# Kernel optimization log

Measured on AMD Instinct MI355X. Metric: run time of the kernel, lower is better.

Reference implementation:

```python
import jax, jax.numpy as jnp
import numpy as np

ANCHORS = np.array([[10,13],[16,30],[33,23],[30,61],[62,45],[59,119],[116,90],[156,198],[373,326]], dtype=np.float32)
ANCHOR_MASK = [[6,7,8],[3,4,5],[0,1,2]]
NUM_CLASSES = 80
IGNORE_THRESH = 0.5
MAX_BOXES = 32   # fixed padding replacing dynamic boolean-mask box extraction
BS = 16
GRIDS = [13, 26, 52]
NA = 3
INPUT = 416.0


def setup_inputs() -> dict:
    rng = np.random.default_rng(0)
    inp = {}
    for l, g in enumerate(GRIDS):
        inp[f"feats{l}"] = jnp.asarray(rng.normal(0.0, 0.5, size=(BS, NA * (5 + NUM_CLASSES), g, g)).astype(np.float32))
        yt = np.zeros((BS, g, g, NA, 5 + NUM_CLASSES), np.float32)
        n_obj = 20
        for b in range(BS):
            gy = rng.integers(0, g, n_obj); gx = rng.integers(0, g, n_obj); a = rng.integers(0, NA, n_obj)
            yt[b, gy, gx, a, 0:2] = rng.uniform(0.0, 1.0, (n_obj, 2)).astype(np.float32)
            yt[b, gy, gx, a, 2:4] = rng.uniform(0.05, 0.5, (n_obj, 2)).astype(np.float32)
            yt[b, gy, gx, a, 4] = 1.0
            cls = rng.integers(0, NUM_CLASSES, n_obj)
            yt[b, gy, gx, a, 5 + cls] = 1.0
        inp[f"ytrue{l}"] = jnp.asarray(yt)
    return inp


def _bce_logits(x, t):
    # BCEWithLogits (stable): softplus(x) - x*t
    return jax.nn.softplus(x) - x * t


def _pairwise_iou(b1, b2):
    # b1: [bs, N, 4] xywh, b2: [bs, M, 4] xywh -> [bs, N, M]
    b1 = b1[:, :, None, :]
    b2 = b2[:, None, :, :]
    b1_mins = b1[..., :2] - b1[..., 2:4] * 0.5
    b1_maxes = b1[..., :2] + b1[..., 2:4] * 0.5
    b2_mins = b2[..., :2] - b2[..., 2:4] * 0.5
    b2_maxes = b2[..., :2] + b2[..., 2:4] * 0.5
    inter_wh = jnp.clip(jnp.minimum(b1_maxes, b2_maxes) - jnp.maximum(b1_mins, b2_mins), 0.0)
    inter = inter_wh[..., 0] * inter_wh[..., 1]
    a1 = b1[..., 2] * b1[..., 3]
    a2 = b2[..., 2] * b2[..., 3]
    return inter / (a1 + a2 - inter)


def _layer_loss(feats, ytrue, anchors):
    bs, _, gh, gw = feats.shape
    C = 5 + NUM_CLASSES
    raw = feats.reshape(bs, NA, C, gh, gw).transpose(0, 3, 4, 1, 2)  # [bs,gh,gw,na,C]
    gy, gx = jnp.meshgrid(jnp.arange(gh), jnp.arange(gw), indexing="ij")
    grid = jnp.stack([gx, gy], axis=-1).astype(raw.dtype)[None, :, :, None, :]  # [1,gh,gw,1,2] (x,y)
    anchors_t = jnp.asarray(anchors, dtype=raw.dtype)                           # [na,2]
    gshape = jnp.array([gh, gw], raw.dtype)

    pred_xy = (jax.nn.sigmoid(raw[..., :2]) + grid) / gshape
    pred_wh = jnp.exp(raw[..., 2:4]) * anchors_t / INPUT
    pred_box = jnp.concatenate([pred_xy, pred_wh], axis=-1)  # [bs,gh,gw,na,4]

    obj = ytrue[..., 4:5]
    raw_true_xy = ytrue[..., :2] * gshape - grid
    safe_wh = jnp.where(obj > 0, ytrue[..., 2:4], anchors_t / INPUT)  # avoids log(0) off-object
    raw_true_wh = jnp.where(obj > 0, jnp.log(safe_wh / anchors_t * INPUT), 0.0)
    box_loss_scale = 2.0 - ytrue[..., 2:3] * ytrue[..., 3:4]

    # --- best-IoU ignore mask (padded, jit-static replacement for per-image boolean masking) ---
    N = gh * gw * NA
    pb = pred_box.reshape(bs, N, 4)
    obj_flat = obj.reshape(bs, N)
    boxes_flat = ytrue[..., :4].reshape(bs, N, 4)
    vals, idx = jax.lax.top_k(obj_flat, MAX_BOXES)                 # obj cells first
    true_boxes = jnp.take_along_axis(boxes_flat, idx[..., None], axis=1)  # [bs,MAXB,4]
    valid = vals > 0.5                                             # [bs,MAXB]
    iou = jnp.where(valid[:, None, :], _pairwise_iou(pb, true_boxes), 0.0)
    best_iou = jnp.max(iou, axis=2).reshape(bs, gh, gw, NA, 1)
    ignore = (best_iou < IGNORE_THRESH).astype(raw.dtype)

    xy_loss = jnp.sum(obj * box_loss_scale * _bce_logits(raw[..., 0:2], raw_true_xy)) / bs
    wh_loss = jnp.sum(obj * box_loss_scale * jnp.square(raw[..., 2:4] - raw_true_wh)) / bs
    conf_bce = _bce_logits(raw[..., 4:5], obj)
    conf_loss = jnp.sum(conf_bce * obj + (1.0 - obj) * conf_bce * ignore) / bs
    cls_loss = jnp.sum(obj * _bce_logits(raw[..., 5:], ytrue[..., 5:])) / bs
    return xy_loss, wh_loss, conf_loss, cls_loss


def reference(feats0, feats1, feats2, ytrue0, ytrue1, ytrue2):
    feats = [feats0, feats1, feats2]
    ytrue = [ytrue0, ytrue1, ytrue2]
    loss_xy = loss_wh = loss_conf = loss_cls = 0.0
    for l in range(3):
        xy, wh, cf, cl = _layer_loss(feats[l], ytrue[l], ANCHORS[ANCHOR_MASK[l]])
        loss_xy = loss_xy + xy
        loss_wh = loss_wh + wh
        loss_conf = loss_conf + cf
        loss_cls = loss_cls + cl
    total = loss_xy + loss_wh + loss_conf + loss_cls
    return (total[None], loss_xy[None], loss_wh[None], loss_conf[None], loss_cls[None])
```

## Files before the change

### kernel.cpp

```cpp
#include <hip/hip_runtime.h>

#define NCLS 80
#define REC  255
#define NA   3
#define BSZ  16
#define MAXB 32

#define G0 13
#define G1 26
#define G2 52
#define GG0 (G0*G0)
#define GG1 (G1*G1)
#define GG2 (G2*G2)
#define CELLS0 (BSZ*NA*GG0)
#define CELLS1 (BSZ*NA*GG1)
#define CELLS2 (BSZ*NA*GG2)
#define TOTAL  (CELLS0+CELLS1+CELLS2)

#define MB ((TOTAL+255)/256)
#define OB 240

__device__ const float d_anch[3][3][2] = {
  {{116.f, 90.f}, {156.f, 198.f}, {373.f, 326.f}},
  {{ 30.f, 61.f}, { 62.f,  45.f}, { 59.f, 119.f}},
  {{ 10.f, 13.f}, { 16.f,  30.f}, { 33.f,  23.f}},
};

__device__ inline float sp(float x) {
  return fmaxf(x, 0.0f) + log1pf(expf(-fabsf(x)));
}
__device__ inline float sigm(float x) { return 1.0f / (1.0f + expf(-x)); }
__device__ inline float wred(float v) {
  #pragma unroll
  for (int off = 32; off > 0; off >>= 1) v += __shfl_down(v, off, 64);
  return v;
}
__device__ inline float wmax(float v) {
  #pragma unroll
  for (int off = 32; off > 0; off >>= 1) v = fmaxf(v, __shfl_xor(v, off, 64));
  return v;
}

__device__ inline int cell_grp(int t) {
  if (t < CELLS0) {
    unsigned r = (unsigned)t / (unsigned)GG0; return (int)(r / 3u);
  } else if (t < CELLS0 + CELLS1) {
    unsigned r = (unsigned)(t - CELLS0) / (unsigned)GG1; return 16 + (int)(r / 3u);
  }
  unsigned r = (unsigned)(t - CELLS0 - CELLS1) / (unsigned)GG2; return 32 + (int)(r / 3u);
}

template<int L>
__device__ inline void gather_one(int idx, const float* __restrict__ yt,
                                  int* __restrict__ cnt, float* __restrict__ boxes,
                                  int* __restrict__ total, int* __restrict__ objlist) {
  constexpr int GG = (L == 0) ? GG0 : (L == 1) ? GG1 : GG2;
  unsigned rest = (unsigned)idx / (unsigned)GG;
  int cell = idx - (int)rest * GG;
  unsigned b = rest / 3u;
  int a = (int)(rest - b * 3u);
  size_t base = ((size_t)((int)b * GG + cell) * 3 + a) * 85;
  float obj = yt[base + 4];
  if (obj > 0.5f) {
    int grp = L * BSZ + (int)b;
    int p = atomicAdd(&cnt[grp], 1);
    if (p < MAXB) {
      float* d = boxes + (grp * MAXB + p) * 4;
      d[0] = yt[base]; d[1] = yt[base + 1]; d[2] = yt[base + 2]; d[3] = yt[base + 3];
    }
    int s = atomicAdd(total, 1);
    if (s < 1024) objlist[s] = (grp << 18) | (a << 16) | cell;
  }
}

__global__ __launch_bounds__(256)
void gather_kernel(const float* __restrict__ y0, const float* __restrict__ y1,
                   const float* __restrict__ y2, int* __restrict__ cnt,
                   float* __restrict__ boxes, int* __restrict__ total,
                   int* __restrict__ objlist) {
  int t = blockIdx.x * 256 + threadIdx.x;
  if (t >= TOTAL) return;
  if (t < CELLS0)               gather_one<0>(t,                   y0, cnt, boxes, total, objlist);
  else if (t < CELLS0 + CELLS1) gather_one<1>(t - CELLS0,          y1, cnt, boxes, total, objlist);
  else                          gather_one<2>(t - CELLS0 - CELLS1, y2, cnt, boxes, total, objlist);
}

template<int L>
__device__ inline float conf_cell(int idx, const float* __restrict__ fp,
                                  const float4* __restrict__ sbox,
                                  const int* __restrict__ scnt, int gmin) {
  constexpr int GG = (L == 0) ? GG0 : (L == 1) ? GG1 : GG2;
  constexpr int G  = (L == 0) ? G0  : (L == 1) ? G1  : G2;
  unsigned rest = (unsigned)idx / (unsigned)GG;
  int cell = idx - (int)rest * GG;
  unsigned b = rest / 3u;
  int a = (int)(rest - b * 3u);
  int fbase = ((int)(b * 3u) + a) * 85 * GG + cell;
  float t0 = fp[fbase];
  float t1 = fp[fbase + GG];
  float t2 = fp[fbase + 2 * GG];
  float t3 = fp[fbase + 3 * GG];
  float t4 = fp[fbase + 4 * GG];
  unsigned yi = (unsigned)cell / (unsigned)G;
  int xi = cell - (int)yi * G;
  float inv_g = 1.0f / (float)G;
  float aw = d_anch[L][a][0], ah = d_anch[L][a][1];
  float px = (sigm(t0) + (float)xi) * inv_g;
  float py = (sigm(t1) + (float)yi) * inv_g;
  float pw = expf(t2) * aw * (1.0f / 416.0f);
  float ph = expf(t3) * ah * (1.0f / 416.0f);
  int si = L * BSZ + (int)b - gmin;
  int nb = scnt[si]; nb = nb > MAXB ? MAXB : nb;
  const float4* bx = sbox + si * MAXB;
  float pminx = px - pw * 0.5f, pmaxx = px + pw * 0.5f;
  float pminy = py - ph * 0.5f, pmaxy = py + ph * 0.5f;
  float pa = pw * ph;
  float best = 0.0f;
  for (int j = 0; j < nb; ++j) {
    float4 tb = bx[j];
    float iw = fminf(pmaxx, tb.x + tb.z * 0.5f) - fmaxf(pminx, tb.x - tb.z * 0.5f);
    float ih = fminf(pmaxy, tb.y + tb.w * 0.5f) - fmaxf(pminy, tb.y - tb.w * 0.5f);
    iw = fmaxf(iw, 0.f); ih = fmaxf(ih, 0.f);
    float inter = iw * ih;
    best = fmaxf(best, inter / (pa + tb.z * tb.w - inter));
  }
  return sp(t4) * (best < 0.5f ? 1.0f : 0.0f);
}

__global__ __launch_bounds__(256)
void loss_kernel(const float* __restrict__ f0, const float* __restrict__ f1,
                 const float* __restrict__ f2, const float* __restrict__ y0,
                 const float* __restrict__ y1, const float* __restrict__ y2,
                 const int* __restrict__ cnt, const float* __restrict__ boxes,
                 const int* __restrict__ total, const int* __restrict__ objlist,
                 float* __restrict__ acc, int* __restrict__ done,
                 float* __restrict__ out) {
  __shared__ float4 sbox[2 * MAXB];
  __shared__ int scnt[2];
  float vxy = 0.f, vwh = 0.f, vconf = 0.f, vcls = 0.f;
  int lane = threadIdx.x & 63, wv = threadIdx.x >> 6;

  if (blockIdx.x < MB) {
    int tfirst = blockIdx.x * 256;
    int tlast  = min(tfirst + 255, TOTAL - 1);
    int gmin = cell_grp(tfirst);
    int ng = cell_grp(tlast) - gmin + 1;
    if (threadIdx.x < ng * MAXB)
      sbox[threadIdx.x] = ((const float4*)boxes)[gmin * MAXB + threadIdx.x];
    if (threadIdx.x < ng) scnt[threadIdx.x] = cnt[gmin + threadIdx.x];
    __syncthreads();
    int t = tfirst + threadIdx.x;
    if (t < TOTAL) {
      if (t < CELLS0)                vconf = conf_cell<0>(t,                   f0, sbox, scnt, gmin);
      else if (t < CELLS0 + CELLS1)  vconf = conf_cell<1>(t - CELLS0,          f1, sbox, scnt, gmin);
      else                           vconf = conf_cell<2>(t - CELLS0 - CELLS1, f2, sbox, scnt, gmin);
    }
  } else {
    int e = (blockIdx.x - MB) * 4 + wv;
    int tot = *total; if (tot > 1024) tot = 1024;
    if (e < tot) {
      int pk = objlist[e];
      int grp = pk >> 18, a = (pk >> 16) & 3, cell = pk & 0xFFFF;
      int l = grp >> 4, b = grp & 15;
      int GGv, Gv;
      const float *fp, *yp;
      if (l == 0)      { GGv = GG0; Gv = G0; fp = f0; yp = y0; }
      else if (l == 1) { GGv = GG1; Gv = G1; fp = f1; yp = y1; }
      else             { GGv = GG2; Gv = G2; fp = f2; yp = y2; }
      int rec   = b * GGv + cell;
      int ybase = rec * REC + a * 85;
      int fbase = (b * NA + a) * 85 * GGv + cell;
      float objv = yp[ybase + 4];

      float lg = fp[fbase + (5 + lane) * GGv];
      vcls = sp(lg) - lg * yp[ybase + 5 + lane];
      if (lane < 16) {
        int c2 = lane + 64;
        float lg2 = fp[fbase + (5 + c2) * GGv];
        vcls += sp(lg2) - lg2 * yp[ybase + 5 + c2];
      }
      vcls *= objv;

      float t0 = fp[fbase];
      float t1 = fp[fbase + GGv];
      float t2 = fp[fbase + 2 * GGv];
      float t3 = fp[fbase + 3 * GGv];
      float t4 = fp[fbase + 4 * GGv];
      int yi = (l == 0) ? cell / G0 : (l == 1) ? cell / G1 : cell / G2;
      int xi = cell - yi * Gv;
      float aw = d_anch[l][a][0], ah = d_anch[l][a][1];
      float px = (sigm(t0) + (float)xi) / (float)Gv;
      float py = (sigm(t1) + (float)yi) / (float)Gv;
      float pw = expf(t2) * aw * (1.0f / 416.0f);
      float ph = expf(t3) * ah * (1.0f / 416.0f);
      int nb = cnt[grp]; nb = nb > MAXB ? MAXB : nb;
      float iou = 0.0f;
      if (lane < nb) {
        float4 tb = ((const float4*)boxes)[grp * MAXB + lane];
        float iw = fminf(px + pw * 0.5f, tb.x + tb.z * 0.5f) - fmaxf(px - pw * 0.5f, tb.x - tb.z * 0.5f);
        float ih = fminf(py + ph * 0.5f, tb.y + tb.w * 0.5f) - fmaxf(py - ph * 0.5f, tb.y - tb.w * 0.5f);
        iw = fmaxf(iw, 0.f); ih = fmaxf(ih, 0.f);
        float inter = iw * ih;
        iou = inter / (pw * ph + tb.z * tb.w - inter);
      }
      float best = wmax(iou);
      if (lane == 0) {
        float ytx = yp[ybase], yty = yp[ybase + 1];
        float ytw = yp[ybase + 2], yth = yp[ybase + 3];
        float rtx = ytx * (float)Gv - (float)xi;
        float rty = yty * (float)Gv - (float)yi;
        float scale = 2.0f - ytw * yth;
        vxy = objv * scale * ((sp(t0) - t0 * rtx) + (sp(t1) - t1 * rty));
        float rtw = logf(ytw * 416.0f / aw);
        float rth = logf(yth * 416.0f / ah);
        vwh = objv * scale * ((t2 - rtw) * (t2 - rtw) + (t3 - rth) * (t3 - rth));
        float ign = best < 0.5f ? 1.0f : 0.0f;
        float spt4 = sp(t4);
        float bce4 = spt4 - t4 * objv;
        vconf = bce4 * (objv + (1.0f - objv) * ign) - spt4 * ign;
      }
    }
  }

  __shared__ float sm[4][4];
  vxy = wred(vxy); vwh = wred(vwh); vconf = wred(vconf); vcls = wred(vcls);
  if (lane == 0) { sm[0][wv] = vxy; sm[1][wv] = vwh; sm[2][wv] = vconf; sm[3][wv] = vcls; }
  __syncthreads();
  if (threadIdx.x < 4) {
    float s = sm[threadIdx.x][0] + sm[threadIdx.x][1] + sm[threadIdx.x][2] + sm[threadIdx.x][3];
    atomicAdd(&acc[threadIdx.x], s);
  }
  __syncthreads();

  if (threadIdx.x == 0) {
    __threadfence();
    int d = atomicAdd(done, 1);
    if (d == (int)gridDim.x - 1) {
      float xy = atomicAdd(&acc[0], 0.0f) * (1.0f / BSZ);
      float wh = atomicAdd(&acc[1], 0.0f) * (1.0f / BSZ);
      float cf = atomicAdd(&acc[2], 0.0f) * (1.0f / BSZ);
      float cl = atomicAdd(&acc[3], 0.0f) * (1.0f / BSZ);
      out[0] = xy + wh + cf + cl;
      out[1] = xy; out[2] = wh; out[3] = cf; out[4] = cl;
    }
  }
}

extern "C" void kernel_launch(void* const* d_in, const int* in_sizes, int n_in,
                              void* d_out, int out_size, void* d_ws, size_t ws_size,
                              hipStream_t stream) {
  const float* f0 = (const float*)d_in[0];
  const float* y0 = (const float*)d_in[1];
  const float* f1 = (const float*)d_in[2];
  const float* y1 = (const float*)d_in[3];
  const float* f2 = (const float*)d_in[4];
  const float* y2 = (const float*)d_in[5];

  float* acc     = (float*)d_ws;
  int*   cnt     = (int*)((char*)d_ws + 64);
  int*   total   = (int*)((char*)d_ws + 256);
  int*   done    = (int*)((char*)d_ws + 260);
  int*   objlist = (int*)((char*)d_ws + 512);
  float* boxes   = (float*)((char*)d_ws + 8192);

  hipMemsetAsync(d_ws, 0, 512, stream);

  gather_kernel<<<MB, 256, 0, stream>>>(y0, y1, y2, cnt, boxes, total, objlist);
  loss_kernel<<<MB + OB, 256, 0, stream>>>(f0, f1, f2, y0, y1, y2,
                                           cnt, boxes, total, objlist,
                                           acc, done, (float*)d_out);
}
```

Before: 171.6 us.

## Fuse memset, gather and loss kernels into one kernel with grid barrier

```diff
diff --git a/kernel.cpp b/kernel.cpp
--- a/kernel.cpp
+++ b/kernel.cpp
@@ -19,6 +19,10 @@
 
 #define MB ((TOTAL+255)/256)
 #define OB 240
+#define NBLK (MB+OB)
+#define MAGIC 0x5EED5EED
+
+#define SCOPE_A __HIP_MEMORY_SCOPE_AGENT
 
 __device__ const float d_anch[3][3][2] = {
   {{116.f, 90.f}, {156.f, 198.f}, {373.f, 326.f}},
@@ -40,6 +44,11 @@
   for (int off = 32; off > 0; off >>= 1) v = fmaxf(v, __shfl_xor(v, off, 64));
   return v;
 }
+
+__device__ inline int   ald (const int* p)   { return __hip_atomic_load((int*)p,   __ATOMIC_RELAXED, SCOPE_A); }
+__device__ inline float aldf(const float* p) { return __hip_atomic_load((float*)p, __ATOMIC_RELAXED, SCOPE_A); }
+__device__ inline void  asti(int* p, int v)     { __hip_atomic_store(p, v, __ATOMIC_RELAXED, SCOPE_A); }
+__device__ inline void  astf(float* p, float v) { __hip_atomic_store(p, v, __ATOMIC_RELAXED, SCOPE_A); }
 
 __device__ inline int cell_grp(int t) {
   if (t < CELLS0) {
@@ -63,26 +72,15 @@
   float obj = yt[base + 4];
   if (obj > 0.5f) {
     int grp = L * BSZ + (int)b;
-    int p = atomicAdd(&cnt[grp], 1);
+    int p = __hip_atomic_fetch_add(&cnt[grp], 1, __ATOMIC_RELAXED, SCOPE_A);
     if (p < MAXB) {
       float* d = boxes + (grp * MAXB + p) * 4;
-      d[0] = yt[base]; d[1] = yt[base + 1]; d[2] = yt[base + 2]; d[3] = yt[base + 3];
-    }
-    int s = atomicAdd(total, 1);
-    if (s < 1024) objlist[s] = (grp << 18) | (a << 16) | cell;
-  }
-}
-
-__global__ __launch_bounds__(256)
-void gather_kernel(const float* __restrict__ y0, const float* __restrict__ y1,
-                   const float* __restrict__ y2, int* __restrict__ cnt,
-                   float* __restrict__ boxes, int* __restrict__ total,
-                   int* __restrict__ objlist) {
-  int t = blockIdx.x * 256 + threadIdx.x;
-  if (t >= TOTAL) return;
-  if (t < CELLS0)               gather_one<0>(t,                   y0, cnt, boxes, total, objlist);
-  else if (t < CELLS0 + CELLS1) gather_one<1>(t - CELLS0,          y1, cnt, boxes, total, objlist);
-  else                          gather_one<2>(t - CELLS0 - CELLS1, y2, cnt, boxes, total, objlist);
+      astf(d + 0, yt[base]);     astf(d + 1, yt[base + 1]);
+      astf(d + 2, yt[base + 2]); astf(d + 3, yt[base + 3]);
+    }
+    int s = __hip_atomic_fetch_add(total, 1, __ATOMIC_RELAXED, SCOPE_A);
+    if (s < 1024) asti(&objlist[s], (grp << 18) | (a << 16) | cell);
+  }
 }
 
 template<int L>
@@ -127,39 +125,78 @@
   return sp(t4) * (best < 0.5f ? 1.0f : 0.0f);
 }
 
-__global__ __launch_bounds__(256)
-void loss_kernel(const float* __restrict__ f0, const float* __restrict__ f1,
-                 const float* __restrict__ f2, const float* __restrict__ y0,
-                 const float* __restrict__ y1, const float* __restrict__ y2,
-                 const int* __restrict__ cnt, const float* __restrict__ boxes,
-                 const int* __restrict__ total, const int* __restrict__ objlist,
-                 float* __restrict__ acc, int* __restrict__ done,
-                 float* __restrict__ out) {
+__global__ __launch_bounds__(256, 4)
+void fused_kernel(const float* __restrict__ f0, const float* __restrict__ f1,
+                  const float* __restrict__ f2, const float* __restrict__ y0,
+                  const float* __restrict__ y1, const float* __restrict__ y2,
+                  float* __restrict__ acc, int* __restrict__ cnt,
+                  int* __restrict__ total, int* __restrict__ done,
+                  int* __restrict__ flag, int* __restrict__ arrive,
+                  int* __restrict__ objlist, float* __restrict__ boxes,
+                  float* __restrict__ out) {
+  const int bid = blockIdx.x;
+  const int tid = threadIdx.x;
+  const int lane = tid & 63, wv = tid >> 6;
+
+  if (tid == 0) {
+    if (bid == 0) {
+      #pragma unroll
+      for (int i = 0; i < 4; ++i) astf(&acc[i], 0.0f);
+      for (int i = 0; i < 48; ++i) asti(&cnt[i], 0);
+      asti(total, 0); asti(done, 0); asti(arrive, 0);
+      __hip_atomic_store(flag, MAGIC, __ATOMIC_RELEASE, SCOPE_A);
+    } else {
+      while (__hip_atomic_load(flag, __ATOMIC_ACQUIRE, SCOPE_A) != MAGIC)
+        __builtin_amdgcn_s_sleep(4);
+    }
+  }
+  __syncthreads();
+
+  {
+    int t = bid * 256 + tid;
+    if (t < TOTAL) {
+      if (t < CELLS0)               gather_one<0>(t,                   y0, cnt, boxes, total, objlist);
+      else if (t < CELLS0 + CELLS1) gather_one<1>(t - CELLS0,          y1, cnt, boxes, total, objlist);
+      else                          gather_one<2>(t - CELLS0 - CELLS1, y2, cnt, boxes, total, objlist);
+    }
+  }
+  __syncthreads();
+
+  if (tid == 0) {
+    __hip_atomic_fetch_add(arrive, 1, __ATOMIC_ACQ_REL, SCOPE_A);
+    while (__hip_atomic_load(arrive, __ATOMIC_ACQUIRE, SCOPE_A) < NBLK)
+      __builtin_amdgcn_s_sleep(4);
+  }
+  __syncthreads();
+
   __shared__ float4 sbox[2 * MAXB];
   __shared__ int scnt[2];
   float vxy = 0.f, vwh = 0.f, vconf = 0.f, vcls = 0.f;
-  int lane = threadIdx.x & 63, wv = threadIdx.x >> 6;
-
-  if (blockIdx.x < MB) {
-    int tfirst = blockIdx.x * 256;
+
+  if (bid < MB) {
+    int tfirst = bid * 256;
     int tlast  = min(tfirst + 255, TOTAL - 1);
     int gmin = cell_grp(tfirst);
     int ng = cell_grp(tlast) - gmin + 1;
-    if (threadIdx.x < ng * MAXB)
-      sbox[threadIdx.x] = ((const float4*)boxes)[gmin * MAXB + threadIdx.x];
-    if (threadIdx.x < ng) scnt[threadIdx.x] = cnt[gmin + threadIdx.x];
+    if (tid < ng * MAXB) {
+      const float* s = boxes + (gmin * MAXB + tid) * 4;
+      float4 v;
+      v.x = aldf(s); v.y = aldf(s + 1); v.z = aldf(s + 2); v.w = aldf(s + 3);
+      sbox[tid] = v;
+    }
+    if (tid < ng) scnt[tid] = ald(&cnt[gmin + tid]);
     __syncthreads();
-    int t = tfirst + threadIdx.x;
+    int t = tfirst + tid;
     if (t < TOTAL) {
       if (t < CELLS0)                vconf = conf_cell<0>(t,                   f0, sbox, scnt, gmin);
       else if (t < CELLS0 + CELLS1)  vconf = conf_cell<1>(t - CELLS0,          f1, sbox, scnt, gmin);
       else                           vconf = conf_cell<2>(t - CELLS0 - CELLS1, f2, sbox, scnt, gmin);
     }
   } else {
-    int e = (blockIdx.x - MB) * 4 + wv;
-    int tot = *total; if (tot > 1024) tot = 1024;
+    int e = (bid - MB) * 4 + wv;
+    int tot = ald(total); if (tot > 1024) tot = 1024;
     if (e < tot) {
-      int pk = objlist[e];
+      int pk = ald(&objlist[e]);
       int grp = pk >> 18, a = (pk >> 16) & 3, cell = pk & 0xFFFF;
       int l = grp >> 4, b = grp & 15;
       int GGv, Gv;
@@ -193,15 +230,16 @@
       float py = (sigm(t1) + (float)yi) / (float)Gv;
       float pw = expf(t2) * aw * (1.0f / 416.0f);
       float ph = expf(t3) * ah * (1.0f / 416.0f);
-      int nb = cnt[grp]; nb = nb > MAXB ? MAXB : nb;
+      int nb = ald(&cnt[grp]); nb = nb > MAXB ? MAXB : nb;
       float iou = 0.0f;
       if (lane < nb) {
-        float4 tb = ((const float4*)boxes)[grp * MAXB + lane];
-        float iw = fminf(px + pw * 0.5f, tb.x + tb.z * 0.5f) - fmaxf(px - pw * 0.5f, tb.x - tb.z * 0.5f);
-        float ih = fminf(py + ph * 0.5f, tb.y + tb.w * 0.5f) - fmaxf(py - ph * 0.5f, tb.y - tb.w * 0.5f);
+        const float* s = boxes + (grp * MAXB + lane) * 4;
+        float bx = aldf(s), by = aldf(s + 1), bz = aldf(s + 2), bw = aldf(s + 3);
+        float iw = fminf(px + pw * 0.5f, bx + bz * 0.5f) - fmaxf(px - pw * 0.5f, bx - bz * 0.5f);
+        float ih = fminf(py + ph * 0.5f, by + bw * 0.5f) - fmaxf(py - ph * 0.5f, by - bw * 0.5f);
         iw = fmaxf(iw, 0.f); ih = fmaxf(ih, 0.f);
         float inter = iw * ih;
-        iou = inter / (pw * ph + tb.z * tb.w - inter);
+        iou = inter / (pw * ph + bz * bw - inter);
       }
       float best = wmax(iou);
       if (lane == 0) {
@@ -226,16 +264,16 @@
   vxy = wred(vxy); vwh = wred(vwh); vconf = wred(vconf); vcls = wred(vcls);
   if (lane == 0) { sm[0][wv] = vxy; sm[1][wv] = vwh; sm[2][wv] = vconf; sm[3][wv] = vcls; }
   __syncthreads();
-  if (threadIdx.x < 4) {
-    float s = sm[threadIdx.x][0] + sm[threadIdx.x][1] + sm[threadIdx.x][2] + sm[threadIdx.x][3];
-    atomicAdd(&acc[threadIdx.x], s);
-  }
-  __syncthreads();
-
-  if (threadIdx.x == 0) {
+  if (tid < 4) {
+    float s = sm[tid][0] + sm[tid][1] + sm[tid][2] + sm[tid][3];
+    atomicAdd(&acc[tid], s);
+  }
+  __syncthreads();
+
+  if (tid == 0) {
     __threadfence();
-    int d = atomicAdd(done, 1);
-    if (d == (int)gridDim.x - 1) {
+    int d = __hip_atomic_fetch_add(done, 1, __ATOMIC_ACQ_REL, SCOPE_A);
+    if (d == NBLK - 1) {
       float xy = atomicAdd(&acc[0], 0.0f) * (1.0f / BSZ);
       float wh = atomicAdd(&acc[1], 0.0f) * (1.0f / BSZ);
       float cf = atomicAdd(&acc[2], 0.0f) * (1.0f / BSZ);
@@ -260,13 +298,12 @@
   int*   cnt     = (int*)((char*)d_ws + 64);
   int*   total   = (int*)((char*)d_ws + 256);
   int*   done    = (int*)((char*)d_ws + 260);
+  int*   flag    = (int*)((char*)d_ws + 264);
+  int*   arrive  = (int*)((char*)d_ws + 268);
   int*   objlist = (int*)((char*)d_ws + 512);
   float* boxes   = (float*)((char*)d_ws + 8192);
 
-  hipMemsetAsync(d_ws, 0, 512, stream);
-
-  gather_kernel<<<MB, 256, 0, stream>>>(y0, y1, y2, cnt, boxes, total, objlist);
-  loss_kernel<<<MB + OB, 256, 0, stream>>>(f0, f1, f2, y0, y1, y2,
-                                           cnt, boxes, total, objlist,
-                                           acc, done, (float*)d_out);
-}
+  fused_kernel<<<NBLK, 256, 0, stream>>>(f0, f1, f2, y0, y1, y2,
+                                         acc, cnt, total, done, flag, arrive,
+                                         objlist, boxes, (float*)d_out);
+}
```

Result: slower. 348.1 us (+102.9%).
